# Kernel optimization log

Measured on AMD Instinct MI355X. Metric: run time of the kernel, lower is better.

The kernel has to match this reference:

```python
import jax, jax.numpy as jnp
import numpy as np
from jax.ops import segment_sum

N = 100000   # nodes
E = 1600000  # edges
D = 128      # node_feature_dim == hidden_dim
DE = 16      # edge_feature_dim
G = 512      # num_graphs
EPS = 1e-5   # BatchNorm eps


def setup_inputs() -> dict:
    key = jax.random.key(0)
    ks = jax.random.split(key, 24)
    inp = {
        "x": jax.random.normal(ks[0], (N, D), jnp.float32),
        "edge_index": jax.random.randint(ks[1], (2, E), 0, N, jnp.int64),
        "batch_idx": jnp.sort(jax.random.randint(ks[2], (N,), 0, G, jnp.int64)),
        "edge_attr": jax.random.normal(ks[3], (E, DE), jnp.float32),
        "num_graphs": G,
    }
    s = 1.0 / np.sqrt(D)
    # GCN layer 1 (D -> D) + BatchNorm1d (eval-mode running stats)
    inp["W1"] = jax.random.normal(ks[4], (D, D), jnp.float32) * s
    inp["b1"] = jnp.zeros((D,), jnp.float32)
    inp["g1"] = jax.random.uniform(ks[5], (D,), jnp.float32, 0.5, 1.5)
    inp["bt1"] = jax.random.normal(ks[6], (D,), jnp.float32) * 0.1
    inp["m1"] = jax.random.normal(ks[7], (D,), jnp.float32) * 0.1
    inp["v1"] = jax.random.uniform(ks[8], (D,), jnp.float32, 0.5, 1.5)
    # GCN layer 2
    inp["W2"] = jax.random.normal(ks[9], (D, D), jnp.float32) * s
    inp["b2"] = jnp.zeros((D,), jnp.float32)
    inp["g2"] = jax.random.uniform(ks[10], (D,), jnp.float32, 0.5, 1.5)
    inp["bt2"] = jax.random.normal(ks[11], (D,), jnp.float32) * 0.1
    inp["m2"] = jax.random.normal(ks[12], (D,), jnp.float32) * 0.1
    inp["v2"] = jax.random.uniform(ks[13], (D,), jnp.float32, 0.5, 1.5)
    # edge encoder: Linear(DE,D) -> ReLU -> Linear(D,D)
    inp["We1"] = jax.random.normal(ks[14], (DE, D), jnp.float32) / np.sqrt(DE)
    inp["be1"] = jnp.zeros((D,), jnp.float32)
    inp["We2"] = jax.random.normal(ks[15], (D, D), jnp.float32) * s
    inp["be2"] = jnp.zeros((D,), jnp.float32)
    return inp


def _gcn_conv(x, W, b, src, dst, n):
    # PyG GCNConv: add self-loops, sym norm D^-1/2 (A+I) D^-1/2, then X W + b
    xw = x @ W  # [n, out]
    loops = jnp.arange(n, dtype=src.dtype)
    s = jnp.concatenate([src, loops])
    d = jnp.concatenate([dst, loops])
    deg = segment_sum(jnp.ones_like(d, dtype=xw.dtype), d, num_segments=n)
    dinv = jnp.where(deg > 0, jax.lax.rsqrt(jnp.maximum(deg, 1.0)), 0.0)
    norm = dinv[s] * dinv[d]  # [e+n]
    msg = xw[s] * norm[:, None]
    return segment_sum(msg, d, num_segments=n) + b


def _bn_relu(x, g, bt, m, v):
    return jax.nn.relu((x - m) * jax.lax.rsqrt(v + EPS) * g + bt)


def reference(x, edge_index, batch_idx, edge_attr, num_graphs,
              W1, b1, g1, bt1, m1, v1,
              W2, b2, g2, bt2, m2, v2,
              We1, be1, We2, be2):
    n = x.shape[0]
    src, dst = edge_index[0], edge_index[1]
    # two GraphConvLayer: GCNConv -> BN(eval) -> ReLU -> Dropout(eval=id)
    h = _bn_relu(_gcn_conv(x, W1, b1, src, dst, n), g1, bt1, m1, v1)
    h = _bn_relu(_gcn_conv(h, W2, b2, src, dst, n), g2, bt2, m2, v2)
    # global mean pool over nodes per graph
    nsum = segment_sum(h, batch_idx, num_segments=num_graphs)
    ncnt = segment_sum(jnp.ones((n,), h.dtype), batch_idx, num_segments=num_graphs)
    graph_repr = nsum / jnp.maximum(ncnt, 1.0)[:, None]
    # edge encoder + per-graph edge mean (fused segment-mean)
    e = jax.nn.relu(edge_attr @ We1 + be1) @ We2 + be2  # [E, D]
    edge_batch = batch_idx[src]
    esum = segment_sum(e, edge_batch, num_segments=num_graphs)
    ecnt = segment_sum(jnp.ones((e.shape[0],), e.dtype), edge_batch, num_segments=num_graphs)
    edge_repr = jnp.where(ecnt[:, None] > 0, esum / jnp.maximum(ecnt, 1.0)[:, None], 0.0)
    return graph_repr + edge_repr
```

## Files before the change

### kernel.cpp

```cpp
#include <hip/hip_runtime.h>

#define N_NODES 100000
#define N_EDGES 1600000
#define D 128
#define DE 16
#define G 512
#define EPSBN 1e-5f
#define ESLICE 4
#define EPB 1024
#define EPT (EPB / 256)
#define SCHUNK 1024
#define NSB ((N_NODES + SCHUNK - 1) / SCHUNK)
#define AGG_CH 16

typedef __bf16 bf16x8 __attribute__((ext_vector_type(8)));
typedef float f32x4 __attribute__((ext_vector_type(4)));

__device__ __forceinline__ float bf_lo(unsigned v) { return __uint_as_float(v << 16); }
__device__ __forceinline__ float bf_hi(unsigned v) { return __uint_as_float(v & 0xffff0000u); }

__global__ void k_init(int* __restrict__ deg, int* __restrict__ ecnt,
                       float* __restrict__ gcnt, float* __restrict__ gsum,
                       float* __restrict__ esum) {
  int i = blockIdx.x * 256 + threadIdx.x;
  if (i < N_NODES) deg[i] = 1;
  if (i < G) { ecnt[i] = 0; gcnt[i] = 0.f; }
  if (i < G * D) { gsum[i] = 0.f; esum[i] = 0.f; }
}

__global__ void k_count(const int* __restrict__ ei, const int* __restrict__ batch,
                        int* __restrict__ deg, int* __restrict__ ecnt) {
  __shared__ int bins[G];
  int tid = threadIdx.x;
  for (int i = tid; i < G; i += 256) bins[i] = 0;
  __syncthreads();
  int base = blockIdx.x * 4096;
  for (int t = tid; t < 4096; t += 256) {
    int e = base + t;
    if (e < N_EDGES) {
      int s = ei[e];
      int d = ei[N_EDGES + e];
      atomicAdd(&deg[d], 1);
      atomicAdd(&bins[batch[s]], 1);
    }
  }
  __syncthreads();
  for (int i = tid; i < G; i += 256) if (bins[i]) atomicAdd(&ecnt[i], bins[i]);
}

__global__ __launch_bounds__(256) void k_scan_part(const int* __restrict__ deg,
                                                   int* __restrict__ part) {
  __shared__ int red[4];
  int tid = threadIdx.x;
  int base = blockIdx.x * SCHUNK + tid * 4;
  int s = 0;
  #pragma unroll
  for (int k = 0; k < 4; ++k) {
    int i = base + k;
    if (i < N_NODES) s += deg[i];
  }
  #pragma unroll
  for (int off = 32; off > 0; off >>= 1) s += __shfl_down(s, off);
  if ((tid & 63) == 0) red[tid >> 6] = s;
  __syncthreads();
  if (tid == 0) part[blockIdx.x] = red[0] + red[1] + red[2] + red[3];
}

__global__ void k_scan_mid(int* __restrict__ part, const int* __restrict__ ecnt,
                           int* __restrict__ ebs, int* __restrict__ ecur_pad) {
  __shared__ int sb[512];
  int tid = threadIdx.x;
  int v = (tid < NSB) ? part[tid] : 0;
  sb[tid] = v;
  __syncthreads();
  for (int off = 1; off < 512; off <<= 1) {
    int t = (tid >= off) ? sb[tid - off] : 0;
    __syncthreads();
    sb[tid] += t;
    __syncthreads();
  }
  if (tid < NSB) part[tid] = sb[tid] - v;
  __syncthreads();
  int v2 = ecnt[tid];
  sb[tid] = v2;
  __syncthreads();
  for (int off = 1; off < 512; off <<= 1) {
    int t = (tid >= off) ? sb[tid - off] : 0;
    __syncthreads();
    sb[tid] += t;
    __syncthreads();
  }
  ebs[tid] = sb[tid] - v2;
  ecur_pad[tid * 16] = sb[tid] - v2;
}

__global__ __launch_bounds__(256) void k_scan_write(const int* __restrict__ deg,
                                                    const int* __restrict__ part,
                                                    int* __restrict__ rs,
                                                    int* __restrict__ cursor,
                                                    float* __restrict__ dinv) {
  __shared__ int sb[256];
  int tid = threadIdx.x;
  int base = blockIdx.x * SCHUNK + tid * 4;
  int d[4];
  int s = 0;
  #pragma unroll
  for (int k = 0; k < 4; ++k) {
    int i = base + k;
    d[k] = (i < N_NODES) ? deg[i] : 0;
    s += d[k];
  }
  sb[tid] = s;
  __syncthreads();
  for (int off = 1; off < 256; off <<= 1) {
    int t = (tid >= off) ? sb[tid - off] : 0;
    __syncthreads();
    sb[tid] += t;
    __syncthreads();
  }
  int ex = sb[tid] - s + part[blockIdx.x];
  #pragma unroll
  for (int k = 0; k < 4; ++k) {
    int i = base + k;
    if (i < N_NODES) {
      rs[i] = ex;
      cursor[i] = ex;
      dinv[i] = rsqrtf((float)d[k]);
      ex += d[k];
    }
  }
}

__global__ __launch_bounds__(256) void k_scatter(const int* __restrict__ ei,
                                                 const int* __restrict__ batch,
                                                 const float* __restrict__ edge_attr,
                                                 int* __restrict__ cursor,
                                                 int* __restrict__ ecur_pad,
                                                 int* __restrict__ nbr,
                                                 __bf16* __restrict__ eaS) {
  __shared__ int bins[G];
  __shared__ int base[G];
  int tid = threadIdx.x;
  for (int i = tid; i < G; i += 256) bins[i] = 0;
  __syncthreads();
  int e0 = blockIdx.x * EPB;
  int ge[EPT], gr[EPT];
  #pragma unroll
  for (int k = 0; k < EPT; ++k) {
    int e = e0 + k * 256 + tid;
    ge[k] = -1;
    if (e < N_EDGES) {
      int s = ei[e], d = ei[N_EDGES + e];
      int pos = atomicAdd(&cursor[d], 1);
      nbr[pos] = s;
      int g = batch[s];
      ge[k] = g;
      gr[k] = atomicAdd(&bins[g], 1);
    }
  }
  __syncthreads();
  for (int i = tid; i < G; i += 256) {
    int cnt = bins[i];
    base[i] = cnt ? atomicAdd(&ecur_pad[i * 16], cnt) : 0;
  }
  __syncthreads();
  #pragma unroll
  for (int k = 0; k < EPT; ++k) {
    if (ge[k] >= 0) {
      int e = e0 + k * 256 + tid;
      int pos = base[ge[k]] + gr[k];
      const float4* p = (const float4*)(edge_attr + (size_t)e * DE);
      float4 f0 = p[0], f1 = p[1], f2 = p[2], f3 = p[3];
      bf16x8 h0, h1;
      h0[0] = (__bf16)f0.x; h0[1] = (__bf16)f0.y; h0[2] = (__bf16)f0.z; h0[3] = (__bf16)f0.w;
      h0[4] = (__bf16)f1.x; h0[5] = (__bf16)f1.y; h0[6] = (__bf16)f1.z; h0[7] = (__bf16)f1.w;
      h1[0] = (__bf16)f2.x; h1[1] = (__bf16)f2.y; h1[2] = (__bf16)f2.z; h1[3] = (__bf16)f2.w;
      h1[4] = (__bf16)f3.x; h1[5] = (__bf16)f3.y; h1[6] = (__bf16)f3.z; h1[7] = (__bf16)f3.w;
      bf16x8* q = (bf16x8*)(eaS + (size_t)pos * DE);
      q[0] = h0; q[1] = h1;
    }
  }
}

__global__ __launch_bounds__(256) void k_gemm_scale(const float* __restrict__ X,
                                                    const float* __restrict__ W,
                                                    const float* __restrict__ dinv,
                                                    __bf16* __restrict__ out) {
  __shared__ float sX[128][32];
  __shared__ float sW[32][128];
  int tid = threadIdx.x;
  int tx = tid & 15, ty = tid >> 4;
  int rowBase = blockIdx.x * 128;
  float acc[8][8] = {};
  for (int kc = 0; kc < 128; kc += 32) {
    #pragma unroll
    for (int i = 0; i < 4; ++i) {
      int idx = tid + i * 256;
      int r = idx >> 3, kq = idx & 7;
      int row = rowBase + r;
      float4 v = make_float4(0.f, 0.f, 0.f, 0.f);
      if (row < N_NODES) v = *(const float4*)(X + (size_t)row * 128 + kc + kq * 4);
      *(float4*)(&sX[r][kq * 4]) = v;
    }
    #pragma unroll
    for (int i = 0; i < 4; ++i) {
      int idx = tid + i * 256;
      int k = idx >> 5, cq = idx & 31;
      *(float4*)(&sW[k][cq * 4]) = *(const float4*)(W + (size_t)(kc + k) * 128 + cq * 4);
    }
    __syncthreads();
    #pragma unroll 4
    for (int k = 0; k < 32; ++k) {
      float a[8], b[8];
      #pragma unroll
      for (int j = 0; j < 8; ++j) a[j] = sX[ty * 8 + j][k];
      *(float4*)(&b[0]) = *(float4*)(&sW[k][tx * 8]);
      *(float4*)(&b[4]) = *(float4*)(&sW[k][tx * 8 + 4]);
      #pragma unroll
      for (int j = 0; j < 8; ++j)
        #pragma unroll
        for (int c = 0; c < 8; ++c) acc[j][c] += a[j] * b[c];
    }
    __syncthreads();
  }
  #pragma unroll
  for (int j = 0; j < 8; ++j) {
    int row = rowBase + ty * 8 + j;
    if (row < N_NODES) {
      float dv = dinv[row];
      bf16x8 o;
      #pragma unroll
      for (int c = 0; c < 8; ++c) o[c] = (__bf16)(acc[j][c] * dv);
      *(bf16x8*)(out + (size_t)row * 128 + tx * 8) = o;
    }
  }
}

__global__ __launch_bounds__(256) void k_agg_bn(const unsigned* __restrict__ Au,
                                                const int* __restrict__ nbr,
                                                const int* __restrict__ rs,
                                                const int* __restrict__ deg,
                                                const float* __restrict__ dinv,
                                                const float* __restrict__ b,
                                                const float* __restrict__ gm,
                                                const float* __restrict__ bt,
                                                const float* __restrict__ m,
                                                const float* __restrict__ v,
                                                float* __restrict__ outB) {
  int tid = threadIdx.x;
  int wave = tid >> 6, lane = tid & 63;
  int c0 = lane * 2, c1 = c0 + 1;
  float sc0 = gm[c0] * rsqrtf(v[c0] + EPSBN), sc1 = gm[c1] * rsqrtf(v[c1] + EPSBN);
  float sh0 = bt[c0] - m[c0] * sc0, sh1 = bt[c1] - m[c1] * sc1;
  float bb0 = b[c0], bb1 = b[c1];
  int base = (blockIdx.x * 4 + wave) * AGG_CH;
  for (int nn = 0; nn < AGG_CH; ++nn) {
    int i = base + nn;
    if (i >= N_NODES) return;
    unsigned sv = Au[(size_t)i * 64 + lane];
    float s0 = bf_lo(sv), s1 = bf_hi(sv);
    int j = rs[i];
    int end = j + deg[i] - 1;
    for (; j + 3 < end; j += 4) {
      int n0 = nbr[j], n1 = nbr[j + 1], n2 = nbr[j + 2], n3 = nbr[j + 3];
      unsigned a0 = Au[(size_t)n0 * 64 + lane];
      unsigned a1 = Au[(size_t)n1 * 64 + lane];
      unsigned a2 = Au[(size_t)n2 * 64 + lane];
      unsigned a3 = Au[(size_t)n3 * 64 + lane];
      s0 += bf_lo(a0) + bf_lo(a1) + bf_lo(a2) + bf_lo(a3);
      s1 += bf_hi(a0) + bf_hi(a1) + bf_hi(a2) + bf_hi(a3);
    }
    for (; j < end; ++j) {
      unsigned a = Au[(size_t)nbr[j] * 64 + lane];
      s0 += bf_lo(a); s1 += bf_hi(a);
    }
    float dv = dinv[i];
    float y0 = fmaxf((dv * s0 + bb0) * sc0 + sh0, 0.f);
    float y1 = fmaxf((dv * s1 + bb1) * sc1 + sh1, 0.f);
    *(float2*)(outB + (size_t)i * 128 + c0) = make_float2(y0, y1);
  }
}

__global__ __launch_bounds__(256) void k_agg_bn_pool(const unsigned* __restrict__ Au,
                                                     const int* __restrict__ nbr,
                                                     const int* __restrict__ rs,
                                                     const int* __restrict__ deg,
                                                     const float* __restrict__ dinv,
                                                     const int* __restrict__ batch,
                                                     const float* __restrict__ b,
                                                     const float* __restrict__ gm,
                                                     const float* __restrict__ bt,
                                                     const float* __restrict__ m,
                                                     const float* __restrict__ v,
                                                     float* __restrict__ gsum,
                                                     float* __restrict__ gcnt) {
  int tid = threadIdx.x;
  int wave = tid >> 6, lane = tid & 63;
  int c0 = lane * 2, c1 = c0 + 1;
  float sc0 = gm[c0] * rsqrtf(v[c0] + EPSBN), sc1 = gm[c1] * rsqrtf(v[c1] + EPSBN);
  float sh0 = bt[c0] - m[c0] * sc0, sh1 = bt[c1] - m[c1] * sc1;
  float bb0 = b[c0], bb1 = b[c1];
  int base = (blockIdx.x * 4 + wave) * AGG_CH;
  if (base >= N_NODES) return;
  float acc0 = 0.f, acc1 = 0.f, cnt = 0.f;
  int curg = -1;
  for (int nn = 0; nn < AGG_CH; ++nn) {
    int i = base + nn;
    if (i >= N_NODES) break;
    int bg = batch[i];
    if (bg != curg) {
      if (curg >= 0) {
        atomicAdd(&gsum[(size_t)curg * 128 + c0], acc0);
        atomicAdd(&gsum[(size_t)curg * 128 + c1], acc1);
        if (lane == 0) atomicAdd(&gcnt[curg], cnt);
      }
      acc0 = 0.f; acc1 = 0.f; cnt = 0.f; curg = bg;
    }
    unsigned sv = Au[(size_t)i * 64 + lane];
    float s0 = bf_lo(sv), s1 = bf_hi(sv);
    int j = rs[i];
    int end = j + deg[i] - 1;
    for (; j + 3 < end; j += 4) {
      int n0 = nbr[j], n1 = nbr[j + 1], n2 = nbr[j + 2], n3 = nbr[j + 3];
      unsigned a0 = Au[(size_t)n0 * 64 + lane];
      unsigned a1 = Au[(size_t)n1 * 64 + lane];
      unsigned a2 = Au[(size_t)n2 * 64 + lane];
      unsigned a3 = Au[(size_t)n3 * 64 + lane];
      s0 += bf_lo(a0) + bf_lo(a1) + bf_lo(a2) + bf_lo(a3);
      s1 += bf_hi(a0) + bf_hi(a1) + bf_hi(a2) + bf_hi(a3);
    }
    for (; j < end; ++j) {
      unsigned a = Au[(size_t)nbr[j] * 64 + lane];
      s0 += bf_lo(a); s1 += bf_hi(a);
    }
    float dv = dinv[i];
    acc0 += fmaxf((dv * s0 + bb0) * sc0 + sh0, 0.f);
    acc1 += fmaxf((dv * s1 + bb1) * sc1 + sh1, 0.f);
    cnt += 1.f;
  }
  if (curg >= 0) {
    atomicAdd(&gsum[(size_t)curg * 128 + c0], acc0);
    atomicAdd(&gsum[(size_t)curg * 128 + c1], acc1);
    if (lane == 0) atomicAdd(&gcnt[curg], cnt);
  }
}

__global__ __launch_bounds__(256) void k_edge_hidden(
    const __bf16* __restrict__ eaS,
    const int* __restrict__ ebs, const int* __restrict__ ecnt,
    const float* __restrict__ We1, const float* __restrict__ be1,
    float* __restrict__ esum) {
  int tid = threadIdx.x;
  int wave = tid >> 6;
  int lane = tid & 63;
  int n = lane & 15;
  int kg = lane >> 4;
  int g = blockIdx.x / ESLICE;
  int slice = blockIdx.x % ESLICE;

  bf16x8 bfrag[8];
  float biasv[8];
  #pragma unroll
  for (int blk = 0; blk < 8; ++blk) {
    #pragma unroll
    for (int j = 0; j < 8; ++j) {
      int k = kg * 8 + j;
      float w = (k < DE) ? We1[k * 128 + blk * 16 + n] : 0.f;
      bfrag[blk][j] = (__bf16)w;
    }
    biasv[blk] = be1[blk * 16 + n];
  }

  int start = ebs[g], cnt = ecnt[g];
  int lim = start + cnt;
  int ntiles = (cnt + 15) >> 4;
  const int nstream = ESLICE * 4;
  int sid = slice * 4 + wave;
  int tpc = (ntiles + nstream - 1) / nstream;
  int t0 = sid * tpc;
  int t1 = t0 + tpc; if (t1 > ntiles) t1 = ntiles;

  float racc[8] = {0.f, 0.f, 0.f, 0.f, 0.f, 0.f, 0.f, 0.f};

  for (int t = t0; t < t1; ++t) {
    int jb = start + (t << 4);
    int row = jb + n;
    int rc = row < lim - 1 ? row : lim - 1;
    bf16x8 afrag = {};
    if (kg < 2) afrag = *(const bf16x8*)(eaS + (size_t)rc * DE + kg * 8);
    bool full = (jb + 16 <= lim);
    if (full) {
      #pragma unroll
      for (int blk = 0; blk < 8; ++blk) {
        f32x4 acc = {0.f, 0.f, 0.f, 0.f};
        acc = __builtin_amdgcn_mfma_f32_16x16x32_bf16(afrag, bfrag[blk], acc, 0, 0, 0);
        #pragma unroll
        for (int r = 0; r < 4; ++r)
          racc[blk] += fmaxf(acc[r] + biasv[blk], 0.f);
      }
    } else {
      #pragma unroll
      for (int blk = 0; blk < 8; ++blk) {
        f32x4 acc = {0.f, 0.f, 0.f, 0.f};
        acc = __builtin_amdgcn_mfma_f32_16x16x32_bf16(afrag, bfrag[blk], acc, 0, 0, 0);
        #pragma unroll
        for (int r = 0; r < 4; ++r) {
          int rr = kg * 4 + r;
          if (jb + rr < lim) racc[blk] += fmaxf(acc[r] + biasv[blk], 0.f);
        }
      }
    }
  }

  #pragma unroll
  for (int blk = 0; blk < 8; ++blk) {
    float vsum = racc[blk];
    vsum += __shfl_xor(vsum, 16);
    vsum += __shfl_xor(vsum, 32);
    if (lane < 16) atomicAdd(&esum[(size_t)g * 128 + blk * 16 + n], vsum);
  }
}

__global__ void k_final(const float* __restrict__ esum, const int* __restrict__ ecnt,
                        const float* __restrict__ gsum, const float* __restrict__ gcnt,
                        const float* __restrict__ We2, const float* __restrict__ be2,
                        float* __restrict__ out) {
  __shared__ float mh[128];
  int g = blockIdx.x, c = threadIdx.x;
  int ec = ecnt[g];
  mh[c] = (ec > 0) ? esum[(size_t)g * 128 + c] / (float)ec : 0.f;
  __syncthreads();
  float acc = 0.f;
  #pragma unroll 8
  for (int k = 0; k < 128; ++k) acc += mh[k] * We2[k * 128 + c];
  float er = (ec > 0) ? (acc + be2[c]) : 0.f;
  float gr = gsum[(size_t)g * 128 + c] / fmaxf(gcnt[g], 1.f);
  out[(size_t)g * 128 + c] = gr + er;
}

extern "C" void kernel_launch(void* const* d_in, const int* in_sizes, int n_in,
                              void* d_out, int out_size, void* d_ws, size_t ws_size,
                              hipStream_t stream) {
  const float* x        = (const float*)d_in[0];
  const int*   ei       = (const int*)d_in[1];
  const int*   batch    = (const int*)d_in[2];
  const float* edge_attr= (const float*)d_in[3];
  const float* W1 = (const float*)d_in[5];
  const float* b1 = (const float*)d_in[6];
  const float* g1 = (const float*)d_in[7];
  const float* bt1= (const float*)d_in[8];
  const float* m1 = (const float*)d_in[9];
  const float* v1 = (const float*)d_in[10];
  const float* W2 = (const float*)d_in[11];
  const float* b2 = (const float*)d_in[12];
  const float* g2 = (const float*)d_in[13];
  const float* bt2= (const float*)d_in[14];
  const float* m2 = (const float*)d_in[15];
  const float* v2 = (const float*)d_in[16];
  const float* We1= (const float*)d_in[17];
  const float* be1= (const float*)d_in[18];
  const float* We2= (const float*)d_in[19];
  const float* be2= (const float*)d_in[20];
  float* out = (float*)d_out;

  char* ws = (char*)d_ws;
  size_t off = 0;
  auto take = [&](size_t bytes) -> char* {
    char* p = ws + off;
    off += (bytes + 255) & ~(size_t)255;
    return p;
  };
  __bf16* A       = (__bf16*)take((size_t)N_NODES * 128 * 2);
  float*  B       = (float*) take((size_t)N_NODES * 128 * 4);
  float*  dinv    = (float*) take((size_t)N_NODES * 4);
  int*    deg     = (int*)   take((size_t)N_NODES * 4);
  int*    rs      = (int*)   take((size_t)N_NODES * 4);
  int*    cursor  = (int*)   take((size_t)N_NODES * 4);
  int*    nbr     = (int*)   take((size_t)(N_EDGES + N_NODES) * 4);
  __bf16* eaS     = (__bf16*)take((size_t)N_EDGES * DE * 2);
  int*    ecnt    = (int*)   take((size_t)G * 4);
  int*    ebs     = (int*)   take((size_t)G * 4);
  int*    ecur_pad= (int*)   take((size_t)G * 16 * 4);
  float*  gcnt    = (float*) take((size_t)G * 4);
  float*  esum    = (float*) take((size_t)G * 128 * 4);
  float*  gsum    = (float*) take((size_t)G * 128 * 4);
  int*    part    = (int*)   take((size_t)NSB * 4);

  k_init<<<(N_NODES + 255) / 256, 256, 0, stream>>>(deg, ecnt, gcnt, gsum, esum);
  k_count<<<(N_EDGES + 4095) / 4096, 256, 0, stream>>>(ei, batch, deg, ecnt);
  k_scan_part<<<NSB, 256, 0, stream>>>(deg, part);
  k_scan_mid<<<1, 512, 0, stream>>>(part, ecnt, ebs, ecur_pad);
  k_scan_write<<<NSB, 256, 0, stream>>>(deg, part, rs, cursor, dinv);
  k_scatter<<<(N_EDGES + EPB - 1) / EPB, 256, 0, stream>>>(ei, batch, edge_attr, cursor, ecur_pad, nbr, eaS);
  const int aggBlocks = (N_NODES + 4 * AGG_CH - 1) / (4 * AGG_CH);
  k_gemm_scale<<<(N_NODES + 127) / 128, 256, 0, stream>>>(x, W1, dinv, A);
  k_agg_bn<<<aggBlocks, 256, 0, stream>>>((const unsigned*)A, nbr, rs, deg, dinv, b1, g1, bt1, m1, v1, B);
  k_gemm_scale<<<(N_NODES + 127) / 128, 256, 0, stream>>>(B, W2, dinv, A);
  k_agg_bn_pool<<<aggBlocks, 256, 0, stream>>>((const unsigned*)A, nbr, rs, deg, dinv, batch, b2, g2, bt2, m2, v2, gsum, gcnt);
  k_edge_hidden<<<G * ESLICE, 256, 0, stream>>>(eaS, ebs, ecnt, We1, be1, esum);
  k_final<<<G, 128, 0, stream>>>(esum, ecnt, gsum, gcnt, We2, be2, out);
}
```

Baseline: 799.8 us.

## Use bf16 MFMA for node GEMMs and two-pass bucketed CSR neighbor build

Replaces the FP32 SIMT 128x128 GEMM with a bf16 MFMA (16x16x32) kernel that uses pre-swizzled weight fragments prepared by a small kernel. It also replaces the per-edge global atomic cursor scatter with a two-pass scheme: edges are first binned by destination bucket into a pairs array, then each bucket's block fills nbr using shared-memory atomics. The aim is to cut FP32 GEMM compute and the scattered global atomic traffic of CSR construction. In exchange it adds an extra pass and a 12.8MB pairs buffer, rounds X to bf16 inside the GEMM, and writes the GEMM output with narrow scalar stores.

```diff
diff --git a/kernel.cpp b/kernel.cpp
--- a/kernel.cpp
+++ b/kernel.cpp
@@ -12,27 +12,34 @@
 #define SCHUNK 1024
 #define NSB ((N_NODES + SCHUNK - 1) / SCHUNK)
 #define AGG_CH 16
+#define DSHIFT 9
+#define DBSZ 512
+#define NBKT ((N_NODES + DBSZ - 1) / DBSZ)
 
 typedef __bf16 bf16x8 __attribute__((ext_vector_type(8)));
+typedef __bf16 bf16x4 __attribute__((ext_vector_type(4)));
 typedef float f32x4 __attribute__((ext_vector_type(4)));
 
 __device__ __forceinline__ float bf_lo(unsigned v) { return __uint_as_float(v << 16); }
 __device__ __forceinline__ float bf_hi(unsigned v) { return __uint_as_float(v & 0xffff0000u); }
 
-__global__ void k_init(int* __restrict__ deg, int* __restrict__ ecnt,
+__global__ void k_init(int* __restrict__ deg, int* __restrict__ ecnt, int* __restrict__ dcnt,
                        float* __restrict__ gcnt, float* __restrict__ gsum,
                        float* __restrict__ esum) {
   int i = blockIdx.x * 256 + threadIdx.x;
   if (i < N_NODES) deg[i] = 1;
   if (i < G) { ecnt[i] = 0; gcnt[i] = 0.f; }
+  if (i < NBKT) dcnt[i] = 0;
   if (i < G * D) { gsum[i] = 0.f; esum[i] = 0.f; }
 }
 
 __global__ void k_count(const int* __restrict__ ei, const int* __restrict__ batch,
-                        int* __restrict__ deg, int* __restrict__ ecnt) {
+                        int* __restrict__ deg, int* __restrict__ ecnt, int* __restrict__ dcnt) {
   __shared__ int bins[G];
+  __shared__ int dbins[NBKT];
   int tid = threadIdx.x;
   for (int i = tid; i < G; i += 256) bins[i] = 0;
+  for (int i = tid; i < NBKT; i += 256) dbins[i] = 0;
   __syncthreads();
   int base = blockIdx.x * 4096;
   for (int t = tid; t < 4096; t += 256) {
@@ -42,10 +49,12 @@
       int d = ei[N_EDGES + e];
       atomicAdd(&deg[d], 1);
       atomicAdd(&bins[batch[s]], 1);
+      atomicAdd(&dbins[d >> DSHIFT], 1);
     }
   }
   __syncthreads();
   for (int i = tid; i < G; i += 256) if (bins[i]) atomicAdd(&ecnt[i], bins[i]);
+  for (int i = tid; i < NBKT; i += 256) if (dbins[i]) atomicAdd(&dcnt[i], dbins[i]);
 }
 
 __global__ __launch_bounds__(256) void k_scan_part(const int* __restrict__ deg,
@@ -67,7 +76,9 @@
 }
 
 __global__ void k_scan_mid(int* __restrict__ part, const int* __restrict__ ecnt,
-                           int* __restrict__ ebs, int* __restrict__ ecur_pad) {
+                           int* __restrict__ ebs, int* __restrict__ ecur_pad,
+                           const int* __restrict__ dcnt, int* __restrict__ dbs,
+                           int* __restrict__ dcur_pad) {
   __shared__ int sb[512];
   int tid = threadIdx.x;
   int v = (tid < NSB) ? part[tid] : 0;
@@ -92,12 +103,22 @@
   }
   ebs[tid] = sb[tid] - v2;
   ecur_pad[tid * 16] = sb[tid] - v2;
+  __syncthreads();
+  int v3 = (tid < NBKT) ? dcnt[tid] : 0;
+  sb[tid] = v3;
+  __syncthreads();
+  for (int off = 1; off < 512; off <<= 1) {
+    int t = (tid >= off) ? sb[tid - off] : 0;
+    __syncthreads();
+    sb[tid] += t;
+    __syncthreads();
+  }
+  if (tid < NBKT) { dbs[tid] = sb[tid] - v3; dcur_pad[tid * 16] = sb[tid] - v3; }
 }
 
 __global__ __launch_bounds__(256) void k_scan_write(const int* __restrict__ deg,
                                                     const int* __restrict__ part,
                                                     int* __restrict__ rs,
-                                                    int* __restrict__ cursor,
                                                     float* __restrict__ dinv) {
   __shared__ int sb[256];
   int tid = threadIdx.x;
@@ -124,7 +145,6 @@
     int i = base + k;
     if (i < N_NODES) {
       rs[i] = ex;
-      cursor[i] = ex;
       dinv[i] = rsqrtf((float)d[k]);
       ex += d[k];
     }
@@ -134,41 +154,49 @@
 __global__ __launch_bounds__(256) void k_scatter(const int* __restrict__ ei,
                                                  const int* __restrict__ batch,
                                                  const float* __restrict__ edge_attr,
-                                                 int* __restrict__ cursor,
                                                  int* __restrict__ ecur_pad,
-                                                 int* __restrict__ nbr,
+                                                 int* __restrict__ dcur_pad,
+                                                 int2* __restrict__ pairs,
                                                  __bf16* __restrict__ eaS) {
-  __shared__ int bins[G];
-  __shared__ int base[G];
-  int tid = threadIdx.x;
-  for (int i = tid; i < G; i += 256) bins[i] = 0;
+  __shared__ int gbins[G];
+  __shared__ int gbase[G];
+  __shared__ int dbins[NBKT];
+  __shared__ int dbase[NBKT];
+  int tid = threadIdx.x;
+  for (int i = tid; i < G; i += 256) gbins[i] = 0;
+  for (int i = tid; i < NBKT; i += 256) dbins[i] = 0;
   __syncthreads();
   int e0 = blockIdx.x * EPB;
-  int ge[EPT], gr[EPT];
+  int ge[EPT], gr[EPT], db[EPT], dr[EPT];
   #pragma unroll
   for (int k = 0; k < EPT; ++k) {
     int e = e0 + k * 256 + tid;
     ge[k] = -1;
     if (e < N_EDGES) {
       int s = ei[e], d = ei[N_EDGES + e];
-      int pos = atomicAdd(&cursor[d], 1);
-      nbr[pos] = s;
       int g = batch[s];
       ge[k] = g;
-      gr[k] = atomicAdd(&bins[g], 1);
+      gr[k] = atomicAdd(&gbins[g], 1);
+      db[k] = d >> DSHIFT;
+      dr[k] = atomicAdd(&dbins[db[k]], 1);
     }
   }
   __syncthreads();
   for (int i = tid; i < G; i += 256) {
-    int cnt = bins[i];
-    base[i] = cnt ? atomicAdd(&ecur_pad[i * 16], cnt) : 0;
+    int cnt = gbins[i];
+    gbase[i] = cnt ? atomicAdd(&ecur_pad[i * 16], cnt) : 0;
+  }
+  for (int i = tid; i < NBKT; i += 256) {
+    int cnt = dbins[i];
+    dbase[i] = cnt ? atomicAdd(&dcur_pad[i * 16], cnt) : 0;
   }
   __syncthreads();
   #pragma unroll
   for (int k = 0; k < EPT; ++k) {
     if (ge[k] >= 0) {
       int e = e0 + k * 256 + tid;
-      int pos = base[ge[k]] + gr[k];
+      int s = ei[e], d = ei[N_EDGES + e];
+      int gpos = gbase[ge[k]] + gr[k];
       const float4* p = (const float4*)(edge_attr + (size_t)e * DE);
       float4 f0 = p[0], f1 = p[1], f2 = p[2], f3 = p[3];
       bf16x8 h0, h1;
@@ -176,62 +204,90 @@
       h0[4] = (__bf16)f1.x; h0[5] = (__bf16)f1.y; h0[6] = (__bf16)f1.z; h0[7] = (__bf16)f1.w;
       h1[0] = (__bf16)f2.x; h1[1] = (__bf16)f2.y; h1[2] = (__bf16)f2.z; h1[3] = (__bf16)f2.w;
       h1[4] = (__bf16)f3.x; h1[5] = (__bf16)f3.y; h1[6] = (__bf16)f3.z; h1[7] = (__bf16)f3.w;
-      bf16x8* q = (bf16x8*)(eaS + (size_t)pos * DE);
+      bf16x8* q = (bf16x8*)(eaS + (size_t)gpos * DE);
       q[0] = h0; q[1] = h1;
-    }
-  }
-}
-
-__global__ __launch_bounds__(256) void k_gemm_scale(const float* __restrict__ X,
-                                                    const float* __restrict__ W,
-                                                    const float* __restrict__ dinv,
-                                                    __bf16* __restrict__ out) {
-  __shared__ float sX[128][32];
-  __shared__ float sW[32][128];
-  int tid = threadIdx.x;
-  int tx = tid & 15, ty = tid >> 4;
-  int rowBase = blockIdx.x * 128;
-  float acc[8][8] = {};
-  for (int kc = 0; kc < 128; kc += 32) {
+      pairs[dbase[db[k]] + dr[k]] = make_int2(s, d);
+    }
+  }
+}
+
+__global__ __launch_bounds__(256) void k_scatter_nbr(const int2* __restrict__ pairs,
+                                                     const int* __restrict__ dbs,
+                                                     const int* __restrict__ dcnt,
+                                                     const int* __restrict__ rs,
+                                                     int* __restrict__ nbr) {
+  __shared__ int cur[DBSZ];
+  int tid = threadIdx.x;
+  int bkt = blockIdx.x;
+  int nodeBase = bkt << DSHIFT;
+  for (int l = tid; l < DBSZ; l += 256) {
+    int node = nodeBase + l;
+    cur[l] = (node < N_NODES) ? rs[node] : 0;
+  }
+  __syncthreads();
+  int start = dbs[bkt], n = dcnt[bkt];
+  for (int i = tid; i < n; i += 256) {
+    int2 p = pairs[start + i];
+    int pos = atomicAdd(&cur[p.y - nodeBase], 1);
+    nbr[pos] = p.x;
+  }
+}
+
+__global__ void k_prep_w(const float* __restrict__ W, __bf16* __restrict__ Wf) {
+  int tid = threadIdx.x;
+  for (int idx = blockIdx.x * 256 + tid; idx < 16384; idx += 8 * 256) {
+    int j = idx & 7;
+    int lane = (idx >> 3) & 63;
+    int cb = (idx >> 9) & 7;
+    int kc = idx >> 12;
+    int k = kc * 32 + (lane >> 4) * 8 + j;
+    int n = cb * 16 + (lane & 15);
+    Wf[idx] = (__bf16)W[k * 128 + n];
+  }
+}
+
+__global__ __launch_bounds__(256) void k_gemm_mfma(const float* __restrict__ X,
+                                                   const __bf16* __restrict__ Wf,
+                                                   const float* __restrict__ dinv,
+                                                   __bf16* __restrict__ out) {
+  __shared__ __bf16 sXb[64][136];
+  int tid = threadIdx.x;
+  int wave = tid >> 6, lane = tid & 63;
+  int m = lane & 15, kg = lane >> 4;
+  int base = blockIdx.x * 64;
+  #pragma unroll
+  for (int i = 0; i < 8; ++i) {
+    int idx = tid + i * 256;
+    int r = idx >> 5, cq = idx & 31;
+    int row = base + r;
+    float4 v = make_float4(0.f, 0.f, 0.f, 0.f);
+    if (row < N_NODES) v = *(const float4*)(X + (size_t)row * 128 + cq * 4);
+    bf16x4 h;
+    h[0] = (__bf16)v.x; h[1] = (__bf16)v.y; h[2] = (__bf16)v.z; h[3] = (__bf16)v.w;
+    *(bf16x4*)(&sXb[r][cq * 4]) = h;
+  }
+  __syncthreads();
+  int r0 = wave * 16;
+  f32x4 acc[8];
+  #pragma unroll
+  for (int cb = 0; cb < 8; ++cb) acc[cb] = (f32x4){0.f, 0.f, 0.f, 0.f};
+  #pragma unroll
+  for (int kc = 0; kc < 4; ++kc) {
+    bf16x8 afrag = *(const bf16x8*)(&sXb[r0 + m][kc * 32 + kg * 8]);
     #pragma unroll
-    for (int i = 0; i < 4; ++i) {
-      int idx = tid + i * 256;
-      int r = idx >> 3, kq = idx & 7;
-      int row = rowBase + r;
-      float4 v = make_float4(0.f, 0.f, 0.f, 0.f);
-      if (row < N_NODES) v = *(const float4*)(X + (size_t)row * 128 + kc + kq * 4);
-      *(float4*)(&sX[r][kq * 4]) = v;
-    }
-    #pragma unroll
-    for (int i = 0; i < 4; ++i) {
-      int idx = tid + i * 256;
-      int k = idx >> 5, cq = idx & 31;
-      *(float4*)(&sW[k][cq * 4]) = *(const float4*)(W + (size_t)(kc + k) * 128 + cq * 4);
-    }
-    __syncthreads();
-    #pragma unroll 4
-    for (int k = 0; k < 32; ++k) {
-      float a[8], b[8];
+    for (int cb = 0; cb < 8; ++cb) {
+      bf16x8 bfrag = *(const bf16x8*)(Wf + (((size_t)(kc * 8 + cb) * 64 + lane) << 3));
+      acc[cb] = __builtin_amdgcn_mfma_f32_16x16x32_bf16(afrag, bfrag, acc[cb], 0, 0, 0);
+    }
+  }
+  #pragma unroll
+  for (int r = 0; r < 4; ++r) {
+    int grow = base + r0 + kg * 4 + r;
+    if (grow < N_NODES) {
+      float dv = dinv[grow];
       #pragma unroll
-      for (int j = 0; j < 8; ++j) a[j] = sX[ty * 8 + j][k];
-      *(float4*)(&b[0]) = *(float4*)(&sW[k][tx * 8]);
-      *(float4*)(&b[4]) = *(float4*)(&sW[k][tx * 8 + 4]);
-      #pragma unroll
-      for (int j = 0; j < 8; ++j)
-        #pragma unroll
-        for (int c = 0; c < 8; ++c) acc[j][c] += a[j] * b[c];
-    }
-    __syncthreads();
-  }
-  #pragma unroll
-  for (int j = 0; j < 8; ++j) {
-    int row = rowBase + ty * 8 + j;
-    if (row < N_NODES) {
-      float dv = dinv[row];
-      bf16x8 o;
-      #pragma unroll
-      for (int c = 0; c < 8; ++c) o[c] = (__bf16)(acc[j][c] * dv);
-      *(bf16x8*)(out + (size_t)row * 128 + tx * 8) = o;
+      for (int cb = 0; cb < 8; ++cb)
+        out[(size_t)grow * 128 + cb * 16 + m] = (__bf16)(acc[cb][r] * dv);
     }
   }
 }
@@ -475,27 +531,35 @@
   float*  dinv    = (float*) take((size_t)N_NODES * 4);
   int*    deg     = (int*)   take((size_t)N_NODES * 4);
   int*    rs      = (int*)   take((size_t)N_NODES * 4);
-  int*    cursor  = (int*)   take((size_t)N_NODES * 4);
   int*    nbr     = (int*)   take((size_t)(N_EDGES + N_NODES) * 4);
+  int2*   pairs   = (int2*)  take((size_t)N_EDGES * 8);
   __bf16* eaS     = (__bf16*)take((size_t)N_EDGES * DE * 2);
+  __bf16* Wf1     = (__bf16*)take((size_t)16384 * 2);
+  __bf16* Wf2     = (__bf16*)take((size_t)16384 * 2);
   int*    ecnt    = (int*)   take((size_t)G * 4);
   int*    ebs     = (int*)   take((size_t)G * 4);
   int*    ecur_pad= (int*)   take((size_t)G * 16 * 4);
+  int*    dcnt    = (int*)   take((size_t)NBKT * 4);
+  int*    dbs     = (int*)   take((size_t)NBKT * 4);
+  int*    dcur_pad= (int*)   take((size_t)NBKT * 16 * 4);
   float*  gcnt    = (float*) take((size_t)G * 4);
   float*  esum    = (float*) take((size_t)G * 128 * 4);
   float*  gsum    = (float*) take((size_t)G * 128 * 4);
   int*    part    = (int*)   take((size_t)NSB * 4);
 
-  k_init<<<(N_NODES + 255) / 256, 256, 0, stream>>>(deg, ecnt, gcnt, gsum, esum);
-  k_count<<<(N_EDGES + 4095) / 4096, 256, 0, stream>>>(ei, batch, deg, ecnt);
+  k_init<<<(N_NODES + 255) / 256, 256, 0, stream>>>(deg, ecnt, dcnt, gcnt, gsum, esum);
+  k_prep_w<<<8, 256, 0, stream>>>(W1, Wf1);
+  k_prep_w<<<8, 256, 0, stream>>>(W2, Wf2);
+  k_count<<<(N_EDGES + 4095) / 4096, 256, 0, stream>>>(ei, batch, deg, ecnt, dcnt);
   k_scan_part<<<NSB, 256, 0, stream>>>(deg, part);
-  k_scan_mid<<<1, 512, 0, stream>>>(part, ecnt, ebs, ecur_pad);
-  k_scan_write<<<NSB, 256, 0, stream>>>(deg, part, rs, cursor, dinv);
-  k_scatter<<<(N_EDGES + EPB - 1) / EPB, 256, 0, stream>>>(ei, batch, edge_attr, cursor, ecur_pad, nbr, eaS);
+  k_scan_mid<<<1, 512, 0, stream>>>(part, ecnt, ebs, ecur_pad, dcnt, dbs, dcur_pad);
+  k_scan_write<<<NSB, 256, 0, stream>>>(deg, part, rs, dinv);
+  k_scatter<<<(N_EDGES + EPB - 1) / EPB, 256, 0, stream>>>(ei, batch, edge_attr, ecur_pad, dcur_pad, pairs, eaS);
+  k_scatter_nbr<<<NBKT, 256, 0, stream>>>(pairs, dbs, dcnt, rs, nbr);
   const int aggBlocks = (N_NODES + 4 * AGG_CH - 1) / (4 * AGG_CH);
-  k_gemm_scale<<<(N_NODES + 127) / 128, 256, 0, stream>>>(x, W1, dinv, A);
+  k_gemm_mfma<<<(N_NODES + 63) / 64, 256, 0, stream>>>(x, Wf1, dinv, A);
   k_agg_bn<<<aggBlocks, 256, 0, stream>>>((const unsigned*)A, nbr, rs, deg, dinv, b1, g1, bt1, m1, v1, B);
-  k_gemm_scale<<<(N_NODES + 127) / 128, 256, 0, stream>>>(B, W2, dinv, A);
+  k_gemm_mfma<<<(N_NODES + 63) / 64, 256, 0, stream>>>(B, Wf2, dinv, A);
   k_agg_bn_pool<<<aggBlocks, 256, 0, stream>>>((const unsigned*)A, nbr, rs, deg, dinv, batch, b2, g2, bt2, m2, v2, gsum, gcnt);
   k_edge_hidden<<<G * ESLICE, 256, 0, stream>>>(eaS, ebs, ecnt, We1, be1, esum);
   k_final<<<G, 128, 0, stream>>>(esum, ecnt, gsum, gcnt, We2, be2, out);
```

Result: faster. 726.8 us (-9.1%).
